# Optimization experiments

Hardware: AMD Instinct MI355X
Metric: run time of the kernel (lower is better)

Reference implementation:

```python
import jax, jax.numpy as jnp
import numpy as np

B, S, T, H, E, VIN, VOUT = 2048, 24, 25, 256, 300, 64, 128


def gru_cell(x, h, Wih, Whh, bih, bhh):
    # PyTorch GRU gate order: r, z, n
    gi = x @ Wih + bih          # [B, 3H]
    gh = h @ Whh + bhh          # [B, 3H]
    hd = h.shape[-1]
    ir, iz, in_ = gi[:, :hd], gi[:, hd:2 * hd], gi[:, 2 * hd:]
    hr, hz, hn = gh[:, :hd], gh[:, hd:2 * hd], gh[:, 2 * hd:]
    r = jax.nn.sigmoid(ir + hr)
    z = jax.nn.sigmoid(iz + hz)
    n = jnp.tanh(in_ + r * hn)
    return (1.0 - z) * n + z * h


def setup_inputs() -> dict:
    key = jax.random.key(0)
    ks = jax.random.split(key, 26)
    it = iter(range(26))

    def p(shape):
        return jax.random.normal(ks[next(it)], shape, jnp.float32) * 0.05

    src = jax.random.randint(ks[next(it)], (S, B), 0, VIN)
    trg = jax.random.randint(ks[next(it)], (T, B), 0, VOUT)
    return dict(
        src=src, trg=trg,
        enc_emb=p((VIN, E)),
        enc_Wih_f=p((E, 3 * H)), enc_Whh_f=p((H, 3 * H)), enc_bih_f=p((3 * H,)), enc_bhh_f=p((3 * H,)),
        enc_Wih_b=p((E, 3 * H)), enc_Whh_b=p((H, 3 * H)), enc_bih_b=p((3 * H,)), enc_bhh_b=p((3 * H,)),
        enc_fcW=p((2 * H, H)), enc_fcb=p((H,)),
        attn_Wh=p((H, H)), attn_We=p((2 * H, H)), attn_b=p((H,)), attn_v=p((H,)),
        dec_emb=p((VOUT, E)),
        dec_Wih=p((E + 2 * H, 3 * H)), dec_Whh=p((H, 3 * H)), dec_bih=p((3 * H,)), dec_bhh=p((3 * H,)),
        fcW=p((H + 2 * H + E, VOUT)), fcb=p((VOUT,)),
        teacher_forcing_ratio=1,
    )


def reference(src, trg, enc_emb, enc_Wih_f, enc_Whh_f, enc_bih_f, enc_bhh_f,
              enc_Wih_b, enc_Whh_b, enc_bih_b, enc_bhh_b, enc_fcW, enc_fcb,
              attn_Wh, attn_We, attn_b, attn_v, dec_emb,
              dec_Wih, dec_Whh, dec_bih, dec_bhh, fcW, fcb,
              teacher_forcing_ratio):
    # ---- Encoder: bidirectional single-layer GRU ----
    x = enc_emb[src]                                   # [S, B, E]
    h0 = jnp.zeros((x.shape[1], H), x.dtype)

    def mk(Wih, Whh, bih, bhh):
        def step(h, xt):
            hn = gru_cell(xt, h, Wih, Whh, bih, bhh)
            return hn, hn
        return step

    hf, out_f = jax.lax.scan(mk(enc_Wih_f, enc_Whh_f, enc_bih_f, enc_bhh_f), h0, x)
    hb, out_b = jax.lax.scan(mk(enc_Wih_b, enc_Whh_b, enc_bih_b, enc_bhh_b), h0, x[::-1])
    enc_out = jnp.concatenate([out_f, out_b[::-1]], axis=-1)   # [S, B, 2H]
    hidden = jnp.tanh(jnp.concatenate([hf, hb], axis=-1) @ enc_fcW + enc_fcb)  # [B, H]

    # ---- Decoder: teacher-forced loop (teacher_forcing_ratio=1 => deterministic) ----
    enc_bse = enc_out.transpose(1, 0, 2)               # [B, S, 2H]
    enc_proj = enc_bse @ attn_We                       # [B, S, H] (hoisted linear part of attn)
    embed_seq = dec_emb[trg[:-1]]                      # [T-1, B, E]

    def dec_step(h, emb_t):
        energy = jnp.tanh((h @ attn_Wh)[:, None, :] + enc_proj + attn_b)  # [B, S, H]
        a = jax.nn.softmax(energy @ attn_v, axis=-1)                      # [B, S]
        weighted = jnp.einsum('bs,bsd->bd', a, enc_bse)                   # [B, 2H]
        xg = jnp.concatenate([emb_t, weighted], axis=-1)                  # [B, E+2H]
        hn = gru_cell(xg, h, dec_Wih, dec_Whh, dec_bih, dec_bhh)          # [B, H]
        logits = jnp.concatenate([hn, weighted, emb_t], axis=-1) @ fcW + fcb
        return hn, logits

    _, logits = jax.lax.scan(dec_step, hidden, embed_seq)  # [T-1, B, VOUT]
    outputs = jnp.concatenate(
        [jnp.zeros((1,) + logits.shape[1:], logits.dtype), logits], axis=0)  # [T, B, VOUT]
    return outputs
```

## Files before the change

### kernel.cpp

```cpp
#include <hip/hip_runtime.h>
#include <hip/hip_bf16.h>

typedef __hip_bfloat16 bf16;
typedef __attribute__((ext_vector_type(8))) short short8;
typedef __attribute__((ext_vector_type(4))) float f32x4;

__device__ __forceinline__ float to_f(float x) { return x; }
__device__ __forceinline__ float to_f(bf16 x) { return __bfloat162float(x); }
__device__ __forceinline__ float ldp(const void* p, size_t i, bool f32) {
  return f32 ? ((const float*)p)[i] : __bfloat162float(((const bf16*)p)[i]);
}
__device__ __forceinline__ short f2b(float f) {
  bf16 h = __float2bfloat16(f);
  return *reinterpret_cast<short*>(&h);
}
__device__ __forceinline__ int perm1024(int c) {
  return ((c & 255) >> 4) * 64 + (c >> 8) * 16 + (c & 15);
}

__global__ void detect_kernel(const void* __restrict__ probe,
                              unsigned* __restrict__ flag) {
  __shared__ int sbad;
  if (threadIdx.x == 0) sbad = 0;
  __syncthreads();
  const unsigned short* u = (const unsigned short*)probe;
  int bad = 0;
  for (int i = threadIdx.x; i < 2048; i += 256) {
    unsigned short w = u[i];
    unsigned e = (w >> 7) & 0xFFu;
    bool plaus = (w == 0) || (w == 0x8000u) || (e >= 0x60u && e <= 0x7Eu);
    if (!plaus) bad++;
  }
  atomicAdd(&sbad, bad);
  __syncthreads();
  if (threadIdx.x == 0) *flag = (sbad > 100) ? 1u : 0u;
}

#define MAXSEG 24
struct PrepArgs {
  int nseg;
  const void* src[MAXSEG];
  long long soff[MAXSEG];
  short* dst[MAXSEG];
  int scols[MAXSEG];
  int dstride[MAXSEG];
  int transp[MAXSEG];
  long long prefix[MAXSEG + 1];
};
__global__ void prep_kernel(PrepArgs a, const unsigned* __restrict__ dflag) {
  const bool isf32 = (*dflag != 0u);
  long long i = (long long)blockIdx.x * 256 + threadIdx.x;
  if (i >= a.prefix[a.nseg]) return;
  int s = 0;
  while (i >= a.prefix[s + 1]) s++;
  long long loc = i - a.prefix[s];
  long long r = loc / a.scols[s], c = loc % a.scols[s];
  float v = a.src[s] ? ldp(a.src[s], (size_t)(a.soff[s] + loc), isf32) : 0.f;
  int tp = a.transp[s];
  long long idx;
  if (tp == 1)
    idx = c * a.dstride[s] + r;
  else if (tp == 2)
    idx = (long long)perm1024((int)c) * a.dstride[s] + r;
  else if (tp == 3)
    idx = perm1024((int)c);
  else
    idx = r * a.dstride[s] + c;
  a.dst[s][idx] = f2b(v);
}

struct GJob {
  const bf16* A;
  const short* WT;
  const bf16* bias;
  float* Cf;
  bf16* Ch;
  const float* Cin;
  const int* cinrow;
  int lda, wst, K, M, N, flags;
};
struct GJobs {
  GJob j[4];
};

__global__ __launch_bounds__(256) void mj_gemm(GJobs args) {
  GJob jb = args.j[blockIdx.z];
  const int n0 = blockIdx.x * 128, m0 = blockIdx.y * 128;
  if (n0 >= jb.N || m0 >= jb.M) return;
  __shared__ short As[128][40];
  __shared__ short Bs[128][40];
  const int tid = threadIdx.x, lane = tid & 63, wave = tid >> 6;
  const int srow = tid >> 1, skoff = (tid & 1) * 16;
  const int wr = (wave >> 1) * 64, wc = (wave & 1) * 64;

  const short* abase =
      (const short*)jb.A + (long long)(m0 + srow) * jb.lda + skoff;
  const short* bbase = jb.WT + (long long)(n0 + srow) * jb.wst + skoff;

  f32x4 acc[4][4];
#pragma unroll
  for (int i = 0; i < 4; i++)
#pragma unroll
    for (int j = 0; j < 4; j++) acc[i][j] = 0.f;

  const int K = jb.K;
  short8 a0 = *(const short8*)(abase);
  short8 a1 = *(const short8*)(abase + 8);
  short8 b0 = *(const short8*)(bbase);
  short8 b1 = *(const short8*)(bbase + 8);

  for (int k0 = 0; k0 < K; k0 += 32) {
    __syncthreads();
    *(short8*)&As[srow][skoff] = a0;
    *(short8*)&As[srow][skoff + 8] = a1;
    *(short8*)&Bs[srow][skoff] = b0;
    *(short8*)&Bs[srow][skoff + 8] = b1;
    __syncthreads();
    int kn = (k0 + 32 < K) ? k0 + 32 : k0;
    a0 = *(const short8*)(abase + kn);
    a1 = *(const short8*)(abase + kn + 8);
    b0 = *(const short8*)(bbase + kn);
    b1 = *(const short8*)(bbase + kn + 8);
    short8 af[4], bfr[4];
#pragma unroll
    for (int i = 0; i < 4; i++)
      af[i] = *(short8*)&As[wr + i * 16 + (lane & 15)][(lane >> 4) * 8];
#pragma unroll
    for (int j = 0; j < 4; j++)
      bfr[j] = *(short8*)&Bs[wc + j * 16 + (lane & 15)][(lane >> 4) * 8];
#pragma unroll
    for (int i = 0; i < 4; i++)
#pragma unroll
      for (int j = 0; j < 4; j++)
        acc[i][j] =
            __builtin_amdgcn_mfma_f32_16x16x32_bf16(af[i], bfr[j], acc[i][j],
                                                    0, 0, 0);
  }

  const int N = jb.N;
  const float* cin = jb.Cin;
  const int* cri = jb.cinrow;
#pragma unroll
  for (int j = 0; j < 4; j++) {
    int col = n0 + wc + j * 16 + (lane & 15);
    float bv = jb.bias ? to_f(jb.bias[col]) : 0.f;
#pragma unroll
    for (int i = 0; i < 4; i++) {
#pragma unroll
      for (int r = 0; r < 4; r++) {
        int row = m0 + wr + i * 16 + (lane >> 4) * 4 + r;
        float v = acc[i][j][r] + bv;
        if (cin) {
          long long crow = cri ? (long long)cri[row] : (long long)row;
          v += cin[crow * N + col];
        }
        if (jb.flags & 4) v = tanhf(v);
        if (jb.Cf) jb.Cf[(long long)row * N + col] = v;
        if (jb.Ch) jb.Ch[(long long)row * N + col] = __float2bfloat16(v);
      }
    }
  }
}

struct CJob {
  const bf16* A;
  const short* WT;
  const bf16* bias;
  const bf16* gh;
  const int* tok;
  const bf16* giTab;
  float* hF;
  bf16* hBf;
  bf16* out2;
  long long out2s;
  int lda, wst, K, hstride, hoff;
};
struct CJobs {
  CJob j[2];
};

__global__ __launch_bounds__(256) void mj_gemm_cell(CJobs args) {
  CJob jb = args.j[blockIdx.z];
  const int n0 = blockIdx.x * 128, m0 = blockIdx.y * 128;
  __shared__ short As[128][40];
  __shared__ short Bs[128][40];
  __shared__ int toks[128];
  const int tid = threadIdx.x, lane = tid & 63, wave = tid >> 6;
  const int srow = tid >> 1, skoff = (tid & 1) * 16;
  const int wr = (wave >> 1) * 64, wcq = (wave & 1) * 64;

  if (tid < 128) toks[tid] = jb.tok[m0 + tid];
  const short* abase =
      (const short*)jb.A + (long long)(m0 + srow) * jb.lda + skoff;
  const short* bbase = jb.WT + (long long)(n0 + srow) * jb.wst + skoff;

  f32x4 acc[4][4];
#pragma unroll
  for (int i = 0; i < 4; i++)
#pragma unroll
    for (int j = 0; j < 4; j++) acc[i][j] = 0.f;

  const int K = jb.K;
  short8 a0 = *(const short8*)(abase);
  short8 a1 = *(const short8*)(abase + 8);
  short8 b0 = *(const short8*)(bbase);
  short8 b1 = *(const short8*)(bbase + 8);

  for (int k0 = 0; k0 < K; k0 += 32) {
    __syncthreads();
    *(short8*)&As[srow][skoff] = a0;
    *(short8*)&As[srow][skoff + 8] = a1;
    *(short8*)&Bs[srow][skoff] = b0;
    *(short8*)&Bs[srow][skoff + 8] = b1;
    __syncthreads();
    int kn = (k0 + 32 < K) ? k0 + 32 : k0;
    a0 = *(const short8*)(abase + kn);
    a1 = *(const short8*)(abase + kn + 8);
    b0 = *(const short8*)(bbase + kn);
    b1 = *(const short8*)(bbase + kn + 8);
    short8 af[4], bfr[4];
#pragma unroll
    for (int i = 0; i < 4; i++)
      af[i] = *(short8*)&As[wr + i * 16 + (lane & 15)][(lane >> 4) * 8];
#pragma unroll
    for (int j = 0; j < 4; j++)
      bfr[j] = *(short8*)&Bs[wcq + j * 16 + (lane & 15)][(lane >> 4) * 8];
#pragma unroll
    for (int i = 0; i < 4; i++)
#pragma unroll
      for (int j = 0; j < 4; j++)
        acc[i][j] =
            __builtin_amdgcn_mfma_f32_16x16x32_bf16(af[i], bfr[j], acc[i][j],
                                                    0, 0, 0);
  }

  const int u = lane & 15, hi4 = (lane >> 4) * 4;
  const int i_h = ((n0 + wcq) >> 6) * 16 + u;
  float b0g = 0.f, b1g = 0.f, b2g = 0.f;
  if (jb.bias) {
    b0g = to_f(jb.bias[n0 + wcq + u]);
    b1g = to_f(jb.bias[n0 + wcq + 16 + u]);
    b2g = to_f(jb.bias[n0 + wcq + 32 + u]);
  }
#pragma unroll
  for (int i = 0; i < 4; i++) {
#pragma unroll
    for (int r = 0; r < 4; r++) {
      int row = m0 + wr + i * 16 + hi4 + r;
      const bf16* gi = jb.giTab + (long long)toks[row - m0] * 768 + i_h;
      float t0 = to_f(gi[0]), t1 = to_f(gi[256]), t2 = to_f(gi[512]);
      float g0 = acc[i][0][r] + b0g, g1 = acc[i][1][r] + b1g,
            g2 = acc[i][2][r] + b2g;
      float ir, iz, in_, hr, hz, hn;
      if (jb.gh) {
        const bf16* gb = jb.gh + (long long)row * 1024 + i_h;
        ir = g0 + t0;
        iz = g1 + t1;
        in_ = g2 + t2;
        hr = to_f(gb[0]);
        hz = to_f(gb[256]);
        hn = to_f(gb[512]);
      } else {
        ir = t0;
        iz = t1;
        in_ = t2;
        hr = g0;
        hz = g1;
        hn = g2;
      }
      long long hidx = (long long)row * jb.hstride + jb.hoff + i_h;
      float hv = jb.hF[hidx];
      float rr = 1.f / (1.f + expf(-(ir + hr)));
      float zz = 1.f / (1.f + expf(-(iz + hz)));
      float nn = tanhf(in_ + rr * hn);
      float o = (1.f - zz) * nn + zz * hv;
      jb.hF[hidx] = o;
      jb.hBf[hidx] = __float2bfloat16(o);
      jb.out2[(long long)row * jb.out2s + i_h] = __float2bfloat16(o);
    }
  }
}

__global__ __launch_bounds__(256) void attn_kernel(
    const bf16* __restrict__ ghw, const bf16* __restrict__ proj,
    const bf16* __restrict__ bse, const void* __restrict__ v,
    bf16* __restrict__ xgc, const unsigned* __restrict__ dflag) {
  const bool isf32 = (*dflag != 0u);
  int b = blockIdx.x, tid = threadIdx.x;
  int wave = tid >> 6, lane = tid & 63;
  __shared__ float partial[24][4];
  __shared__ float aw[24];
  float vh = to_f(ghw[(long long)b * 1024 + 768 + tid]);
  float vv = ldp(v, tid, isf32);
  const bf16* pb = proj + (long long)b * 24 * 256;
#pragma unroll 4
  for (int s = 0; s < 24; s++) {
    float e = tanhf(vh + __bfloat162float(pb[s * 256 + tid]));
    float t = vv * e;
#pragma unroll
    for (int off = 32; off > 0; off >>= 1) t += __shfl_down(t, off, 64);
    if (lane == 0) partial[s][wave] = t;
  }
  __syncthreads();
  if (tid == 0) {
    float sc[24];
    float mx = -1e30f;
    for (int s = 0; s < 24; s++) {
      float xv = partial[s][0] + partial[s][1] + partial[s][2] + partial[s][3];
      sc[s] = xv;
      mx = fmaxf(mx, xv);
    }
    float sum = 0.f;
    for (int s = 0; s < 24; s++) {
      sc[s] = expf(sc[s] - mx);
      sum += sc[s];
    }
    float inv = 1.f / sum;
    for (int s = 0; s < 24; s++) aw[s] = sc[s] * inv;
  }
  __syncthreads();
  const bf16* eb = bse + (long long)b * 24 * 512;
  float w0 = 0.f, w1 = 0.f;
#pragma unroll 4
  for (int s = 0; s < 24; s++) {
    float a = aw[s];
    w0 += a * __bfloat162float(eb[s * 512 + tid]);
    w1 += a * __bfloat162float(eb[s * 512 + 256 + tid]);
  }
  bf16* xb = xgc + (long long)b * 768;
  xb[tid] = __float2bfloat16(w0);
  xb[256 + tid] = __float2bfloat16(w1);
}

__global__ void sentinel_kernel(float* out, int n) {
  int i = blockIdx.x * 256 + threadIdx.x;
  if (i < n) out[i] = 123.0f;
}

extern "C" void kernel_launch(void* const* d_in, const int* in_sizes, int n_in,
                              void* d_out, int out_size, void* d_ws,
                              size_t ws_size, hipStream_t stream) {
  const int B = 2048, S = 24, T = 25, VOUT = 128;
  const int* src = (const int*)d_in[0];
  const int* trg = (const int*)d_in[1];
  const void* enc_emb = d_in[2];
  const void* enc_Wih_f = d_in[3];
  const void* enc_Whh_f = d_in[4];
  const void* enc_bih_f = d_in[5];
  const void* enc_bhh_f = d_in[6];
  const void* enc_Wih_b = d_in[7];
  const void* enc_Whh_b = d_in[8];
  const void* enc_bih_b = d_in[9];
  const void* enc_bhh_b = d_in[10];
  const void* enc_fcW = d_in[11];
  const void* enc_fcb = d_in[12];
  const void* attn_Wh = d_in[13];
  const void* attn_We = d_in[14];
  const void* attn_b = d_in[15];
  const void* attn_v = d_in[16];
  const void* dec_emb = d_in[17];
  const void* dec_Wih = d_in[18];
  const void* dec_Whh = d_in[19];
  const void* dec_bih = d_in[20];
  const void* dec_bhh = d_in[21];
  const void* fcW = d_in[22];
  const void* fcb = d_in[23];
  float* out = (float*)d_out;

  size_t need = 0;
  auto place = [&](size_t bytes) {
    size_t off = need;
    need += (bytes + 255) & ~(size_t)255;
    return off;
  };
  size_t o_flag = place(256);
  size_t o_wstart = need;
  size_t oEmbE = place(64 * 320 * 2);
  size_t oEmbD = place(128 * 320 * 2);
  size_t oWT1 = place(768 * 320 * 2);
  size_t oWT2 = place(1024 * 256 * 2);
  size_t oWT3 = place(768 * 320 * 2);
  size_t oWT4 = place(1024 * 256 * 2);
  size_t oWT5 = place(256 * 512 * 2);
  size_t oWT6 = place(256 * 512 * 2);
  size_t oWcT = place(1024 * 256 * 2);
  size_t oW7aT = place(768 * 320 * 2);
  size_t oW7bT = place(1024 * 512 * 2);
  size_t oW8aT = place(128 * 320 * 2);
  size_t oW8bT = place(128 * 768 * 2);
  size_t oB1 = place(768 * 2), oB2 = place(1024 * 2);
  size_t oB3 = place(768 * 2), oB4 = place(1024 * 2);
  size_t oB5 = place(256 * 2), oB6 = place(256 * 2);
  size_t oB7 = place(768 * 2), oBc = place(1024 * 2), oB8 = place(128 * 2);
  size_t o_wend = need;
  size_t o_bse = place((size_t)B * S * 512 * 2);
  size_t o_proj = place((size_t)B * S * 256 * 2);
  size_t o_ghw = place((size_t)B * 1024 * 2);
  size_t o_hfb = place((size_t)B * 512 * 4);
  size_t o_hb0 = place((size_t)B * 512 * 2);
  size_t o_hb1 = place((size_t)B * 512 * 2);
  size_t o_hd = place((size_t)B * 256 * 4);
  size_t o_hdbf = place((size_t)B * 256 * 2);
  size_t o_xgc = place((size_t)(T - 1) * B * 768 * 2);
  size_t o_gtF = place(128 * 768 * 2);
  size_t o_gtB = place(128 * 768 * 2);
  size_t o_gtE = place(128 * 768 * 2);
  size_t o_fcT = place(128 * 128 * 4);

  if (ws_size < need) {
    sentinel_kernel<<<(out_size + 255) / 256, 256, 0, stream>>>(out, out_size);
    return;
  }

  char* base = (char*)d_ws;
  unsigned* dflag = (unsigned*)(base + o_flag);
  bf16* embE = (bf16*)(base + oEmbE);
  bf16* embD = (bf16*)(base + oEmbD);
  short* WT1 = (short*)(base + oWT1);
  short* WT2p = (short*)(base + oWT2);
  short* WT3 = (short*)(base + oWT3);
  short* WT4p = (short*)(base + oWT4);
  short* WT5 = (short*)(base + oWT5);
  short* WT6 = (short*)(base + oWT6);
  short* WcT = (short*)(base + oWcT);
  short* W7aT = (short*)(base + oW7aT);
  short* W7bTp = (short*)(base + oW7bT);
  short* W8aT = (short*)(base + oW8aT);
  short* W8bT = (short*)(base + oW8bT);
  bf16 *B1 = (bf16*)(base + oB1), *B2p = (bf16*)(base + oB2);
  bf16 *B3 = (bf16*)(base + oB3), *B4p = (bf16*)(base + oB4);
  bf16 *B5 = (bf16*)(base + oB5), *B6 = (bf16*)(base + oB6);
  bf16 *B7 = (bf16*)(base + oB7), *Bc = (bf16*)(base + oBc);
  bf16* B8 = (bf16*)(base + oB8);
  bf16* bse = (bf16*)(base + o_bse);
  bf16* proj = (bf16*)(base + o_proj);
  bf16* ghw = (bf16*)(base + o_ghw);
  float* hfb = (float*)(base + o_hfb);
  bf16* hb[2] = {(bf16*)(base + o_hb0), (bf16*)(base + o_hb1)};
  float* h_d = (float*)(base + o_hd);
  bf16* hdbf = (bf16*)(base + o_hdbf);
  bf16* xgcAll = (bf16*)(base + o_xgc);
  bf16* giTabF = (bf16*)(base + o_gtF);
  bf16* giTabB = (bf16*)(base + o_gtB);
  bf16* giTabE = (bf16*)(base + o_gtE);
  float* fcTab = (float*)(base + o_fcT);

  detect_kernel<<<1, 256, 0, stream>>>(enc_emb, dflag);
  (void)hipMemsetAsync(base + o_wstart, 0, o_wend - o_wstart, stream);

  PrepArgs pa;
  int ns = 0;
  long long tot = 0;
  auto seg = [&](const void* s, long long soff, short* dst, int scols,
                 int dstride, int transp, long long count) {
    pa.src[ns] = s;
    pa.soff[ns] = soff;
    pa.dst[ns] = dst;
    pa.scols[ns] = scols;
    pa.dstride[ns] = dstride;
    pa.transp[ns] = transp;
    pa.prefix[ns] = tot;
    tot += count;
    ns++;
  };
  seg(enc_emb, 0, (short*)embE, 300, 320, 0, 64 * 300);
  seg(dec_emb, 0, (short*)embD, 300, 320, 0, 128 * 300);
  seg(enc_Wih_f, 0, WT1, 768, 320, 1, 230400);
  seg(enc_Whh_f, 0, WT2p, 768, 256, 2, 196608);
  seg(enc_Wih_b, 0, WT3, 768, 320, 1, 230400);
  seg(enc_Whh_b, 0, WT4p, 768, 256, 2, 196608);
  seg(enc_fcW, 0, WT5, 256, 512, 1, 131072);
  seg(attn_We, 0, WT6, 256, 512, 1, 131072);
  seg(dec_Whh, 0, WcT, 768, 256, 1, 196608);
  seg(attn_Wh, 0, WcT + 768 * 256, 256, 256, 1, 65536);
  seg(dec_Wih, 0, W7aT, 768, 320, 1, 300 * 768);
  seg(dec_Wih, (long long)300 * 768, W7bTp, 768, 512, 2, 512 * 768);
  seg(fcW, (long long)768 * 128, W8aT, 128, 320, 1, 300 * 128);
  seg(fcW, (long long)256 * 128, W8bT, 128, 768, 1, 512 * 128);
  seg(fcW, 0, W8bT + 512, 128, 768, 1, 256 * 128);
  seg(enc_bih_f, 0, (short*)B1, 768, 768, 0, 768);
  seg(enc_bhh_f, 0, (short*)B2p, 768, 1024, 3, 768);
  seg(enc_bih_b, 0, (short*)B3, 768, 768, 0, 768);
  seg(enc_bhh_b, 0, (short*)B4p, 768, 1024, 3, 768);
  seg(enc_fcb, 0, (short*)B5, 256, 256, 0, 256);
  seg(attn_b, 0, (short*)B6, 256, 256, 0, 256);
  seg(dec_bih, 0, (short*)B7, 768, 768, 0, 768);
  seg(dec_bhh, 0, (short*)Bc, 768, 768, 0, 768);
  seg(fcb, 0, (short*)B8, 128, 128, 0, 128);
  pa.prefix[ns] = tot;
  pa.nseg = ns;
  prep_kernel<<<(int)((tot + 255) / 256), 256, 0, stream>>>(pa, dflag);

  (void)hipMemsetAsync(hfb, 0, (size_t)B * 512 * 4, stream);
  (void)hipMemsetAsync(hb[0], 0, (size_t)B * 512 * 2, stream);
  (void)hipMemsetAsync(out, 0, (size_t)B * VOUT * 4, stream);

  auto launch = [&](const GJob* jobs, int nj, int gx, int gy) {
    GJobs a{};
    for (int i = 0; i < nj; i++) a.j[i] = jobs[i];
    mj_gemm<<<dim3(gx, gy, nj), 256, 0, stream>>>(a);
  };
  auto launchC = [&](const CJob* jobs, int nj) {
    CJobs a{};
    for (int i = 0; i < nj; i++) a.j[i] = jobs[i];
    mj_gemm_cell<<<dim3(8, 16, nj), 256, 0, stream>>>(a);
  };

  {
    GJob tj[4];
    tj[0] = {embE, WT1, B1, nullptr, giTabF, nullptr, nullptr,
             320, 320, 320, 128, 768, 0};
    tj[1] = {embE, WT3, B3, nullptr, giTabB, nullptr, nullptr,
             320, 320, 320, 128, 768, 0};
    tj[2] = {embD, W7aT, B7, nullptr, giTabE, nullptr, nullptr,
             320, 320, 320, 128, 768, 0};
    tj[3] = {embD, W8aT, B8, fcTab, nullptr, nullptr, nullptr,
             320, 320, 320, 128, 128, 0};
    launch(tj, 4, 6, 1);
  }

  for (int s = 0; s < S; s++) {
    CJob c[2];
    c[0] = {hb[s & 1], WT2p, B2p, nullptr, src + (size_t)s * B, giTabF,
            hfb, hb[(s + 1) & 1], bse + (size_t)s * 512, 12288,
            512, 256, 256, 512, 0};
    c[1] = {hb[s & 1] + 256, WT4p, B4p, nullptr,
            src + (size_t)(S - 1 - s) * B, giTabB,
            hfb, hb[(s + 1) & 1], bse + (size_t)(S - 1 - s) * 512 + 256, 12288,
            512, 256, 256, 512, 256};
    launchC(c, 2);
  }

  {
    GJob mj[2];
    mj[0] = {hb[0], WT5, B5, h_d, hdbf, nullptr, nullptr,
             512, 512, 512, B, 256, 4};
    mj[1] = {bse, WT6, B6, nullptr, proj, nullptr, nullptr,
             512, 512, 512, B * S, 256, 0};
    launch(mj, 2, 2, 384);
  }

  auto wc_job = [&]() -> GJob {
    return {hdbf, WcT, Bc, nullptr, ghw, nullptr, nullptr,
            256, 256, 256, B, 1024, 0};
  };
  {
    GJob j0 = wc_job();
    launch(&j0, 1, 8, 16);
  }
  for (int t = 0; t < T - 1; t++) {
    bf16* xr = xgcAll + (size_t)t * B * 768;
    attn_kernel<<<B, 256, 0, stream>>>(ghw, proj, bse, attn_v, xr, dflag);
    CJob c = {xr, W7bTp, nullptr, ghw, trg + (size_t)t * B, giTabE,
              h_d, hdbf, xr + 512, 768, 768, 512, 512, 256, 0};
    launchC(&c, 1);
    if (t < T - 2) {
      GJob j0 = wc_job();
      launch(&j0, 1, 8, 16);
    }
  }
  {
    GJob jf = {xgcAll, W8bT, nullptr, out + (size_t)B * VOUT, nullptr,
               fcTab, trg, 768, 768, 768, (T - 1) * B, 128, 0};
    launch(&jf, 1, 1, 384);
  }
}
```

Measured before the change: 2.190 ms.

## Fuse decoder hidden GEMM into attention and GRU cell kernels per step

Removes the separate per-step h@[Whh|Wh] GEMM launch in the decoder. The attention kernel now computes h@attn_Wh itself with a per-block dot product over a shared-memory copy of h. The cell kernel computes both the input-side and hidden-side GEMMs in a single block, which is why the hidden state is now double-buffered. This saves one launch and the ghw round-trip per step. In exchange, each attention block re-reads the full 256x256 Wh matrix through scalar FMAs rather than MFMA, which could cost more than it saves.

```diff
diff --git a/kernel.cpp b/kernel.cpp
--- a/kernel.cpp
+++ b/kernel.cpp
@@ -4,6 +4,9 @@
 typedef __hip_bfloat16 bf16;
 typedef __attribute__((ext_vector_type(8))) short short8;
 typedef __attribute__((ext_vector_type(4))) float f32x4;
+
+#define MFMA(va, vb, vc) \
+  __builtin_amdgcn_mfma_f32_16x16x32_bf16(va, vb, vc, 0, 0, 0)
 
 __device__ __forceinline__ float to_f(float x) { return x; }
 __device__ __forceinline__ float to_f(bf16 x) { return __bfloat162float(x); }
@@ -13,6 +16,12 @@
 __device__ __forceinline__ short f2b(float f) {
   bf16 h = __float2bfloat16(f);
   return *reinterpret_cast<short*>(&h);
+}
+__device__ __forceinline__ float b2f(short s_) {
+  unsigned int ui = ((unsigned int)(unsigned short)s_) << 16;
+  float f;
+  __builtin_memcpy(&f, &ui, 4);
+  return f;
 }
 __device__ __forceinline__ int perm1024(int c) {
   return ((c & 255) >> 4) * 64 + (c >> 8) * 16 + (c & 15);
@@ -96,27 +105,24 @@
   const short* abase =
       (const short*)jb.A + (long long)(m0 + srow) * jb.lda + skoff;
   const short* bbase = jb.WT + (long long)(n0 + srow) * jb.wst + skoff;
-
   f32x4 acc[4][4];
 #pragma unroll
   for (int i = 0; i < 4; i++)
 #pragma unroll
     for (int j = 0; j < 4; j++) acc[i][j] = 0.f;
 
-  const int K = jb.K;
   short8 a0 = *(const short8*)(abase);
   short8 a1 = *(const short8*)(abase + 8);
   short8 b0 = *(const short8*)(bbase);
   short8 b1 = *(const short8*)(bbase + 8);
-
-  for (int k0 = 0; k0 < K; k0 += 32) {
+  for (int k0 = 0; k0 < jb.K; k0 += 32) {
     __syncthreads();
     *(short8*)&As[srow][skoff] = a0;
     *(short8*)&As[srow][skoff + 8] = a1;
     *(short8*)&Bs[srow][skoff] = b0;
     *(short8*)&Bs[srow][skoff + 8] = b1;
     __syncthreads();
-    int kn = (k0 + 32 < K) ? k0 + 32 : k0;
+    int kn = (k0 + 32 < jb.K) ? k0 + 32 : k0;
     a0 = *(const short8*)(abase + kn);
     a1 = *(const short8*)(abase + kn + 8);
     b0 = *(const short8*)(bbase + kn);
@@ -131,12 +137,8 @@
 #pragma unroll
     for (int i = 0; i < 4; i++)
 #pragma unroll
-      for (int j = 0; j < 4; j++)
-        acc[i][j] =
-            __builtin_amdgcn_mfma_f32_16x16x32_bf16(af[i], bfr[j], acc[i][j],
-                                                    0, 0, 0);
-  }
-
+      for (int j = 0; j < 4; j++) acc[i][j] = MFMA(af[i], bfr[j], acc[i][j]);
+  }
   const int N = jb.N;
   const float* cin = jb.Cin;
   const int* cri = jb.cinrow;
@@ -166,7 +168,6 @@
   const bf16* A;
   const short* WT;
   const bf16* bias;
-  const bf16* gh;
   const int* tok;
   const bf16* giTab;
   float* hF;
@@ -200,20 +201,18 @@
 #pragma unroll
     for (int j = 0; j < 4; j++) acc[i][j] = 0.f;
 
-  const int K = jb.K;
   short8 a0 = *(const short8*)(abase);
   short8 a1 = *(const short8*)(abase + 8);
   short8 b0 = *(const short8*)(bbase);
   short8 b1 = *(const short8*)(bbase + 8);
-
-  for (int k0 = 0; k0 < K; k0 += 32) {
+  for (int k0 = 0; k0 < jb.K; k0 += 32) {
     __syncthreads();
     *(short8*)&As[srow][skoff] = a0;
     *(short8*)&As[srow][skoff + 8] = a1;
     *(short8*)&Bs[srow][skoff] = b0;
     *(short8*)&Bs[srow][skoff + 8] = b1;
     __syncthreads();
-    int kn = (k0 + 32 < K) ? k0 + 32 : k0;
+    int kn = (k0 + 32 < jb.K) ? k0 + 32 : k0;
     a0 = *(const short8*)(abase + kn);
     a1 = *(const short8*)(abase + kn + 8);
     b0 = *(const short8*)(bbase + kn);
@@ -228,46 +227,24 @@
 #pragma unroll
     for (int i = 0; i < 4; i++)
 #pragma unroll
-      for (int j = 0; j < 4; j++)
-        acc[i][j] =
-            __builtin_amdgcn_mfma_f32_16x16x32_bf16(af[i], bfr[j], acc[i][j],
-                                                    0, 0, 0);
+      for (int j = 0; j < 4; j++) acc[i][j] = MFMA(af[i], bfr[j], acc[i][j]);
   }
 
   const int u = lane & 15, hi4 = (lane >> 4) * 4;
   const int i_h = ((n0 + wcq) >> 6) * 16 + u;
-  float b0g = 0.f, b1g = 0.f, b2g = 0.f;
-  if (jb.bias) {
-    b0g = to_f(jb.bias[n0 + wcq + u]);
-    b1g = to_f(jb.bias[n0 + wcq + 16 + u]);
-    b2g = to_f(jb.bias[n0 + wcq + 32 + u]);
-  }
+  const float b0g = to_f(jb.bias[n0 + wcq + u]);
+  const float b1g = to_f(jb.bias[n0 + wcq + 16 + u]);
+  const float b2g = to_f(jb.bias[n0 + wcq + 32 + u]);
 #pragma unroll
   for (int i = 0; i < 4; i++) {
 #pragma unroll
     for (int r = 0; r < 4; r++) {
       int row = m0 + wr + i * 16 + hi4 + r;
       const bf16* gi = jb.giTab + (long long)toks[row - m0] * 768 + i_h;
-      float t0 = to_f(gi[0]), t1 = to_f(gi[256]), t2 = to_f(gi[512]);
-      float g0 = acc[i][0][r] + b0g, g1 = acc[i][1][r] + b1g,
-            g2 = acc[i][2][r] + b2g;
-      float ir, iz, in_, hr, hz, hn;
-      if (jb.gh) {
-        const bf16* gb = jb.gh + (long long)row * 1024 + i_h;
-        ir = g0 + t0;
-        iz = g1 + t1;
-        in_ = g2 + t2;
-        hr = to_f(gb[0]);
-        hz = to_f(gb[256]);
-        hn = to_f(gb[512]);
-      } else {
-        ir = t0;
-        iz = t1;
-        in_ = t2;
-        hr = g0;
-        hz = g1;
-        hn = g2;
-      }
+      float ir = to_f(gi[0]), iz = to_f(gi[256]), in_ = to_f(gi[512]);
+      float hr = acc[i][0][r] + b0g;
+      float hz = acc[i][1][r] + b1g;
+      float hn = acc[i][2][r] + b2g;
       long long hidx = (long long)row * jb.hstride + jb.hoff + i_h;
       float hv = jb.hF[hidx];
       float rr = 1.f / (1.f + expf(-(ir + hr)));
@@ -281,21 +258,38 @@
   }
 }
 
-__global__ __launch_bounds__(256) void attn_kernel(
-    const bf16* __restrict__ ghw, const bf16* __restrict__ proj,
-    const bf16* __restrict__ bse, const void* __restrict__ v,
-    bf16* __restrict__ xgc, const unsigned* __restrict__ dflag) {
-  const bool isf32 = (*dflag != 0u);
+struct A2Args {
+  const bf16* h;
+  const short* WhT;
+  const bf16* proj;
+  const bf16* bse;
+  const void* v;
+  const unsigned* dflag;
+  bf16* xr;
+};
+__global__ __launch_bounds__(256) void attn2_kernel(A2Args a) {
   int b = blockIdx.x, tid = threadIdx.x;
   int wave = tid >> 6, lane = tid & 63;
+  __shared__ short hsh[256];
   __shared__ float partial[24][4];
   __shared__ float aw[24];
-  float vh = to_f(ghw[(long long)b * 1024 + 768 + tid]);
-  float vv = ldp(v, tid, isf32);
-  const bf16* pb = proj + (long long)b * 24 * 256;
+  const bool isf32 = (*a.dflag != 0u);
+  hsh[tid] = ((const short*)a.h)[(long long)b * 256 + tid];
+  float vv = ldp(a.v, tid, isf32);
+  __syncthreads();
+  float hw = 0.f;
+  const short* wrow = a.WhT + (size_t)tid * 256;
+#pragma unroll 8
+  for (int kt = 0; kt < 32; kt++) {
+    short8 w8 = *(const short8*)(wrow + kt * 8);
+    short8 h8 = *(const short8*)&hsh[kt * 8];
+#pragma unroll
+    for (int e = 0; e < 8; e++) hw += b2f(h8[e]) * b2f(w8[e]);
+  }
+  const bf16* pb = a.proj + (long long)b * 24 * 256;
 #pragma unroll 4
   for (int s = 0; s < 24; s++) {
-    float e = tanhf(vh + __bfloat162float(pb[s * 256 + tid]));
+    float e = tanhf(hw + to_f(pb[s * 256 + tid]));
     float t = vv * e;
 #pragma unroll
     for (int off = 32; off > 0; off >>= 1) t += __shfl_down(t, off, 64);
@@ -319,17 +313,120 @@
     for (int s = 0; s < 24; s++) aw[s] = sc[s] * inv;
   }
   __syncthreads();
-  const bf16* eb = bse + (long long)b * 24 * 512;
+  const bf16* eb = a.bse + (long long)b * 24 * 512;
   float w0 = 0.f, w1 = 0.f;
 #pragma unroll 4
   for (int s = 0; s < 24; s++) {
-    float a = aw[s];
-    w0 += a * __bfloat162float(eb[s * 512 + tid]);
-    w1 += a * __bfloat162float(eb[s * 512 + 256 + tid]);
-  }
-  bf16* xb = xgc + (long long)b * 768;
+    float aa = aw[s];
+    w0 += aa * to_f(eb[s * 512 + tid]);
+    w1 += aa * to_f(eb[s * 512 + 256 + tid]);
+  }
+  bf16* xb = a.xr + (long long)b * 768;
   xb[tid] = __float2bfloat16(w0);
   xb[256 + tid] = __float2bfloat16(w1);
+}
+
+struct C2Args {
+  const bf16* xr;
+  const bf16* hprev;
+  const short* W7p;
+  const short* WhhP;
+  const bf16* bhhP;
+  const int* tok;
+  const bf16* giTabE;
+  float* hF;
+  bf16* hnext;
+  bf16* xout;
+};
+
+__device__ __forceinline__ void tile_acc3(const short* abase,
+                                          const short* bbase, int K,
+                                          short (*As)[40], short (*Bs)[40],
+                                          int srow, int skoff, int wr,
+                                          int wcq, int lane, f32x4 acc[4][3]) {
+  short8 a0 = *(const short8*)(abase);
+  short8 a1 = *(const short8*)(abase + 8);
+  short8 b0 = *(const short8*)(bbase);
+  short8 b1 = *(const short8*)(bbase + 8);
+  for (int k0 = 0; k0 < K; k0 += 32) {
+    __syncthreads();
+    *(short8*)&As[srow][skoff] = a0;
+    *(short8*)&As[srow][skoff + 8] = a1;
+    *(short8*)&Bs[srow][skoff] = b0;
+    *(short8*)&Bs[srow][skoff + 8] = b1;
+    __syncthreads();
+    int kn = (k0 + 32 < K) ? k0 + 32 : k0;
+    a0 = *(const short8*)(abase + kn);
+    a1 = *(const short8*)(abase + kn + 8);
+    b0 = *(const short8*)(bbase + kn);
+    b1 = *(const short8*)(bbase + kn + 8);
+    short8 af[4], bfr[3];
+#pragma unroll
+    for (int i = 0; i < 4; i++)
+      af[i] = *(short8*)&As[wr + i * 16 + (lane & 15)][(lane >> 4) * 8];
+#pragma unroll
+    for (int j = 0; j < 3; j++)
+      bfr[j] = *(short8*)&Bs[wcq + j * 16 + (lane & 15)][(lane >> 4) * 8];
+#pragma unroll
+    for (int i = 0; i < 4; i++)
+#pragma unroll
+      for (int j = 0; j < 3; j++) acc[i][j] = MFMA(af[i], bfr[j], acc[i][j]);
+  }
+}
+
+__global__ __launch_bounds__(256) void cell2_kernel(C2Args a) {
+  const int n0 = blockIdx.x * 128, m0 = blockIdx.y * 128;
+  __shared__ short As[128][40];
+  __shared__ short Bs[128][40];
+  __shared__ int toks[128];
+  const int tid = threadIdx.x, lane = tid & 63, wave = tid >> 6;
+  const int srow = tid >> 1, skoff = (tid & 1) * 16;
+  const int wr = (wave >> 1) * 64, wcq = (wave & 1) * 64;
+  if (tid < 128) toks[tid] = a.tok[m0 + tid];
+
+  f32x4 accA[4][3], accB[4][3];
+#pragma unroll
+  for (int i = 0; i < 4; i++)
+#pragma unroll
+    for (int j = 0; j < 3; j++) {
+      accA[i][j] = 0.f;
+      accB[i][j] = 0.f;
+    }
+  tile_acc3((const short*)a.xr + (long long)(m0 + srow) * 768 + skoff,
+            a.W7p + (long long)(n0 + srow) * 512 + skoff, 512, As, Bs, srow,
+            skoff, wr, wcq, lane, accA);
+  tile_acc3((const short*)a.hprev + (long long)(m0 + srow) * 256 + skoff,
+            a.WhhP + (long long)(n0 + srow) * 256 + skoff, 256, As, Bs, srow,
+            skoff, wr, wcq, lane, accB);
+
+  const int u = lane & 15, hi4 = (lane >> 4) * 4;
+  const int i_h = ((n0 + wcq) >> 6) * 16 + u;
+  const float b0g = to_f(a.bhhP[n0 + wcq + u]);
+  const float b1g = to_f(a.bhhP[n0 + wcq + 16 + u]);
+  const float b2g = to_f(a.bhhP[n0 + wcq + 32 + u]);
+#pragma unroll
+  for (int i = 0; i < 4; i++) {
+#pragma unroll
+    for (int r = 0; r < 4; r++) {
+      int row = m0 + wr + i * 16 + hi4 + r;
+      const bf16* gi = a.giTabE + (long long)toks[row - m0] * 768 + i_h;
+      float ir = accA[i][0][r] + to_f(gi[0]);
+      float iz = accA[i][1][r] + to_f(gi[256]);
+      float in_ = accA[i][2][r] + to_f(gi[512]);
+      float hr = accB[i][0][r] + b0g;
+      float hz = accB[i][1][r] + b1g;
+      float hn = accB[i][2][r] + b2g;
+      long long hidx = (long long)row * 256 + i_h;
+      float hv = a.hF[hidx];
+      float rr = 1.f / (1.f + expf(-(ir + hr)));
+      float zz = 1.f / (1.f + expf(-(iz + hz)));
+      float nn = tanhf(in_ + rr * hn);
+      float o = (1.f - zz) * nn + zz * hv;
+      a.hF[hidx] = o;
+      a.hnext[hidx] = __float2bfloat16(o);
+      a.xout[(long long)row * 768 + 512 + i_h] = __float2bfloat16(o);
+    }
+  }
 }
 
 __global__ void sentinel_kernel(float* out, int n) {
@@ -383,7 +480,8 @@
   size_t oWT4 = place(1024 * 256 * 2);
   size_t oWT5 = place(256 * 512 * 2);
   size_t oWT6 = place(256 * 512 * 2);
-  size_t oWcT = place(1024 * 256 * 2);
+  size_t oWhhP = place(1024 * 256 * 2);
+  size_t oWhT = place(256 * 256 * 2);
   size_t oW7aT = place(768 * 320 * 2);
   size_t oW7bT = place(1024 * 512 * 2);
   size_t oW8aT = place(128 * 320 * 2);
@@ -391,17 +489,17 @@
   size_t oB1 = place(768 * 2), oB2 = place(1024 * 2);
   size_t oB3 = place(768 * 2), oB4 = place(1024 * 2);
   size_t oB5 = place(256 * 2), oB6 = place(256 * 2);
-  size_t oB7 = place(768 * 2), oBc = place(1024 * 2), oB8 = place(128 * 2);
+  size_t oB7 = place(768 * 2), oBcP = place(1024 * 2), oB8 = place(128 * 2);
   size_t o_wend = need;
   size_t o_bse = place((size_t)B * S * 512 * 2);
   size_t o_proj = place((size_t)B * S * 256 * 2);
-  size_t o_ghw = place((size_t)B * 1024 * 2);
+  size_t o_xgc = place((size_t)(T - 1) * B * 768 * 2);
   size_t o_hfb = place((size_t)B * 512 * 4);
   size_t o_hb0 = place((size_t)B * 512 * 2);
   size_t o_hb1 = place((size_t)B * 512 * 2);
   size_t o_hd = place((size_t)B * 256 * 4);
-  size_t o_hdbf = place((size_t)B * 256 * 2);
-  size_t o_xgc = place((size_t)(T - 1) * B * 768 * 2);
+  size_t o_hdb0 = place((size_t)B * 256 * 2);
+  size_t o_hdb1 = place((size_t)B * 256 * 2);
   size_t o_gtF = place(128 * 768 * 2);
   size_t o_gtB = place(128 * 768 * 2);
   size_t o_gtE = place(128 * 768 * 2);
@@ -422,7 +520,8 @@
   short* WT4p = (short*)(base + oWT4);
   short* WT5 = (short*)(base + oWT5);
   short* WT6 = (short*)(base + oWT6);
-  short* WcT = (short*)(base + oWcT);
+  short* WhhP = (short*)(base + oWhhP);
+  short* WhT = (short*)(base + oWhT);
   short* W7aT = (short*)(base + oW7aT);
   short* W7bTp = (short*)(base + oW7bT);
   short* W8aT = (short*)(base + oW8aT);
@@ -430,16 +529,15 @@
   bf16 *B1 = (bf16*)(base + oB1), *B2p = (bf16*)(base + oB2);
   bf16 *B3 = (bf16*)(base + oB3), *B4p = (bf16*)(base + oB4);
   bf16 *B5 = (bf16*)(base + oB5), *B6 = (bf16*)(base + oB6);
-  bf16 *B7 = (bf16*)(base + oB7), *Bc = (bf16*)(base + oBc);
+  bf16 *B7 = (bf16*)(base + oB7), *BcP = (bf16*)(base + oBcP);
   bf16* B8 = (bf16*)(base + oB8);
   bf16* bse = (bf16*)(base + o_bse);
   bf16* proj = (bf16*)(base + o_proj);
-  bf16* ghw = (bf16*)(base + o_ghw);
+  bf16* xgcAll = (bf16*)(base + o_xgc);
   float* hfb = (float*)(base + o_hfb);
   bf16* hb[2] = {(bf16*)(base + o_hb0), (bf16*)(base + o_hb1)};
   float* h_d = (float*)(base + o_hd);
-  bf16* hdbf = (bf16*)(base + o_hdbf);
-  bf16* xgcAll = (bf16*)(base + o_xgc);
+  bf16* hdbf[2] = {(bf16*)(base + o_hdb0), (bf16*)(base + o_hdb1)};
   bf16* giTabF = (bf16*)(base + o_gtF);
   bf16* giTabB = (bf16*)(base + o_gtB);
   bf16* giTabE = (bf16*)(base + o_gtE);
@@ -471,8 +569,8 @@
   seg(enc_Whh_b, 0, WT4p, 768, 256, 2, 196608);
   seg(enc_fcW, 0, WT5, 256, 512, 1, 131072);
   seg(attn_We, 0, WT6, 256, 512, 1, 131072);
-  seg(dec_Whh, 0, WcT, 768, 256, 1, 196608);
-  seg(attn_Wh, 0, WcT + 768 * 256, 256, 256, 1, 65536);
+  seg(dec_Whh, 0, WhhP, 768, 256, 2, 196608);
+  seg(attn_Wh, 0, WhT, 256, 256, 1, 65536);
   seg(dec_Wih, 0, W7aT, 768, 320, 1, 300 * 768);
   seg(dec_Wih, (long long)300 * 768, W7bTp, 768, 512, 2, 512 * 768);
   seg(fcW, (long long)768 * 128, W8aT, 128, 320, 1, 300 * 128);
@@ -485,7 +583,7 @@
   seg(enc_fcb, 0, (short*)B5, 256, 256, 0, 256);
   seg(attn_b, 0, (short*)B6, 256, 256, 0, 256);
   seg(dec_bih, 0, (short*)B7, 768, 768, 0, 768);
-  seg(dec_bhh, 0, (short*)Bc, 768, 768, 0, 768);
+  seg(dec_bhh, 0, (short*)BcP, 768, 1024, 3, 768);
   seg(fcb, 0, (short*)B8, 128, 128, 0, 128);
   pa.prefix[ns] = tot;
   pa.nseg = ns;
@@ -499,11 +597,6 @@
     GJobs a{};
     for (int i = 0; i < nj; i++) a.j[i] = jobs[i];
     mj_gemm<<<dim3(gx, gy, nj), 256, 0, stream>>>(a);
-  };
-  auto launchC = [&](const CJob* jobs, int nj) {
-    CJobs a{};
-    for (int i = 0; i < nj; i++) a.j[i] = jobs[i];
-    mj_gemm_cell<<<dim3(8, 16, nj), 256, 0, stream>>>(a);
   };
 
   {
@@ -520,45 +613,35 @@
   }
 
   for (int s = 0; s < S; s++) {
-    CJob c[2];
-    c[0] = {hb[s & 1], WT2p, B2p, nullptr, src + (size_t)s * B, giTabF,
-            hfb, hb[(s + 1) & 1], bse + (size_t)s * 512, 12288,
-            512, 256, 256, 512, 0};
-    c[1] = {hb[s & 1] + 256, WT4p, B4p, nullptr,
-            src + (size_t)(S - 1 - s) * B, giTabB,
-            hfb, hb[(s + 1) & 1], bse + (size_t)(S - 1 - s) * 512 + 256, 12288,
-            512, 256, 256, 512, 256};
-    launchC(c, 2);
+    CJobs ca{};
+    ca.j[0] = {hb[s & 1], WT2p, B2p, src + (size_t)s * B, giTabF,
+               hfb, hb[(s + 1) & 1], bse + (size_t)s * 512, 12288,
+               512, 256, 256, 512, 0};
+    ca.j[1] = {hb[s & 1] + 256, WT4p, B4p, src + (size_t)(S - 1 - s) * B,
+               giTabB, hfb, hb[(s + 1) & 1],
+               bse + (size_t)(S - 1 - s) * 512 + 256, 12288,
+               512, 256, 256, 512, 256};
+    mj_gemm_cell<<<dim3(8, 16, 2), 256, 0, stream>>>(ca);
   }
 
   {
     GJob mj[2];
-    mj[0] = {hb[0], WT5, B5, h_d, hdbf, nullptr, nullptr,
+    mj[0] = {hb[0], WT5, B5, h_d, hdbf[0], nullptr, nullptr,
              512, 512, 512, B, 256, 4};
     mj[1] = {bse, WT6, B6, nullptr, proj, nullptr, nullptr,
              512, 512, 512, B * S, 256, 0};
     launch(mj, 2, 2, 384);
   }
 
-  auto wc_job = [&]() -> GJob {
-    return {hdbf, WcT, Bc, nullptr, ghw, nullptr, nullptr,
-            256, 256, 256, B, 1024, 0};
-  };
-  {
-    GJob j0 = wc_job();
-    launch(&j0, 1, 8, 16);
-  }
   for (int t = 0; t < T - 1; t++) {
     bf16* xr = xgcAll + (size_t)t * B * 768;
-    attn_kernel<<<B, 256, 0, stream>>>(ghw, proj, bse, attn_v, xr, dflag);
-    CJob c = {xr, W7bTp, nullptr, ghw, trg + (size_t)t * B, giTabE,
-              h_d, hdbf, xr + 512, 768, 768, 512, 512, 256, 0};
-    launchC(&c, 1);
-    if (t < T - 2) {
-      GJob j0 = wc_job();
-      launch(&j0, 1, 8, 16);
-    }
-  }
+    A2Args aa{hdbf[t & 1], WhT, proj, bse, attn_v, dflag, xr};
+    attn2_kernel<<<B, 256, 0, stream>>>(aa);
+    C2Args cc{xr,    hdbf[t & 1], W7bTp, WhhP, BcP,
+              trg + (size_t)t * B, giTabE, h_d, hdbf[(t + 1) & 1], xr};
+    cell2_kernel<<<dim3(8, 16), 256, 0, stream>>>(cc);
+  }
+
   {
     GJob jf = {xgcAll, W8bT, nullptr, out + (size_t)B * VOUT, nullptr,
                fcTab, trg, 768, 768, 768, (T - 1) * B, 128, 0};
```

Result: slower. 2.676 ms (+22.2%).
